# Performance work log

Hardware: AMD Instinct MI355X
Metric: run time of the kernel (lower is better)

The kernel has to match this reference:

```python
import jax, jax.numpy as jnp
import numpy as np
from jax.scipy.linalg import solve_triangular

JITTER = 1e-4  # settings.jitter
N, NUM_NODES, DIN, DOUT, M, DEG = 2048, 64, 4, 4, 128, 8
P = DEG * DIN  # parent-feature width per node


def _rbf(a, b):
    # unit-variance, unit-lengthscale RBF kernel: [Na, D] x [Nb, D] -> [Na, Nb]
    sq = (jnp.sum(a * a, -1)[:, None] + jnp.sum(b * b, -1)[None, :]
          - 2.0 * (a @ b.T))
    return jnp.exp(-0.5 * jnp.maximum(sq, 0.0))


def setup_inputs() -> dict:
    key = jax.random.key(0)
    k1, k2, k3, k4 = jax.random.split(key, 4)
    X = jax.random.normal(k1, (N, NUM_NODES * DIN), jnp.float32)
    Z = jax.random.normal(k2, (M, NUM_NODES * DIN), jnp.float32)
    q_mu = 0.1 * jax.random.normal(k3, (M, NUM_NODES * DOUT), jnp.float32)
    q_sqrt = (0.05 * jax.random.normal(k4, (NUM_NODES, DOUT, M, M), jnp.float32)
              + jnp.eye(M, dtype=jnp.float32))
    # fixed-degree graph: parents of node nd are (nd+k) % NUM_NODES, k<DEG;
    # pa[nd] holds the DIN contiguous feature columns of each parent (as in pa_idx)
    parents = (np.arange(NUM_NODES)[:, None] + np.arange(DEG)[None, :]) % NUM_NODES
    cols = (parents[:, :, None] * DIN + np.arange(DIN)[None, None, :]).reshape(NUM_NODES, P)
    pa = jnp.asarray(cols, dtype=jnp.int32)
    return {"X": X, "Z": Z, "q_mu": q_mu, "q_sqrt": q_sqrt, "pa": pa}


def reference(X, Z, q_mu, q_sqrt, pa):
    num_nodes, dout, m, _ = q_sqrt.shape
    n = X.shape[0]
    eye = jnp.eye(m, dtype=X.dtype)
    # q_mu columns per node: [M, nodes*Dout] -> [nodes, M, Dout]
    q_mu_n = q_mu.reshape(m, num_nodes, dout).transpose(1, 0, 2)

    def per_node(pa_nd, qmu_nd, qs_nd):
        Zn = Z[:, pa_nd]             # [M, P]
        Xn = X[:, pa_nd]             # [N, P]
        Ku = _rbf(Zn, Zn) + JITTER * eye
        Lu = jnp.linalg.cholesky(Ku)
        Kuf = _rbf(Zn, Xn)           # [M, N]
        A = solve_triangular(Lu, Kuf, lower=True)
        A = solve_triangular(Lu.T, A, lower=False)   # Kuu^{-1} Kuf, [M, N]
        mean = A.T @ qmu_nd          # [N, Dout] (Zero mean function)
        Lq = jnp.tril(qs_nd)         # [Dout, M, M]
        SK = jnp.einsum('dij,dkj->dik', Lq, Lq) - Ku[None]  # S - Kuu
        B = jnp.einsum('dmk,kn->dmn', SK, A)                 # [Dout, M, N]
        delta = jnp.einsum('mn,dmn->dn', A, B)               # [Dout, N]
        var = 1.0 + delta.T          # Kdiag of unit-variance RBF is 1
        return mean, var

    mean, var = jax.vmap(per_node)(pa, q_mu_n, q_sqrt)   # [nodes, N, Dout]
    mean = mean.transpose(1, 0, 2).reshape(n, num_nodes * dout)
    var = var.transpose(1, 0, 2).reshape(n, num_nodes * dout)
    return mean, var
```

## Files before the change

### kernel.cpp

```cpp
#include <hip/hip_runtime.h>
#include <hip/hip_bf16.h>

#define NN      2048
#define NODES   64
#define DIN     4
#define DOUT    4
#define MM      128
#define DEG     8
#define PP      32
#define JITTER  1e-4f

typedef __attribute__((ext_vector_type(8))) short short8;
typedef __attribute__((ext_vector_type(4))) float f32x4;
typedef __attribute__((ext_vector_type(4))) unsigned short bf16x4;

#define HSTRIDE 98304

__device__ __forceinline__ unsigned short f2b(float f) {
    union { float f; unsigned int u; } v; v.f = f;
    unsigned int u = v.u;
    u += 0x7fffu + ((u >> 16) & 1u);
    return (unsigned short)(u >> 16);
}
__device__ __forceinline__ float b2f(unsigned short h) {
    union { unsigned int u; float f; } v; v.u = ((unsigned int)h) << 16;
    return v.f;
}
__device__ __forceinline__ short8 pack8(f32x4 a, f32x4 b, float& sq) {
    short8 r;
    #pragma unroll
    for (int e = 0; e < 4; e++) {
        unsigned short ha = f2b(a[e]), hb = f2b(b[e]);
        float fa = b2f(ha), fb = b2f(hb);
        sq += fa * fa + fb * fb;
        r[e] = (short)ha; r[e + 4] = (short)hb;
    }
    return r;
}

__device__ __forceinline__ void gload16(const unsigned short* g, unsigned short* l) {
    __builtin_amdgcn_global_load_lds(
        (const __attribute__((address_space(1))) unsigned int*)g,
        (__attribute__((address_space(3))) unsigned int*)l, 16, 0, 0);
}

__global__ __launch_bounds__(512) void k_ns(const float* __restrict__ Z,
                                            const int* __restrict__ pa,
                                            const float* __restrict__ qmu,
                                            unsigned short* __restrict__ Wbf,
                                            unsigned short* __restrict__ Hbuf,
                                            unsigned short* __restrict__ Zpan,
                                            float* __restrict__ zsqg) {
    __shared__ unsigned short As[16384];
    __shared__ unsigned short Bs[16384];
    __shared__ float zsqs[128];
    __shared__ int cols[32];
    int node = blockIdx.x, t = threadIdx.x;
    int wv = t >> 6, ln = t & 63;
    if (t < 32) cols[t] = pa[node * 32 + t];
    __syncthreads();

    int wmI = wv & 1, wnI = wv >> 1;
    int wm = wmI * 64, wn = wnI * 32;
    int lr = ln & 15, lk = ln >> 4;
    int cg0 = cols[lk * 8], cg1 = cols[lk * 8 + 4];

    short8 zv[4], xv[2];
    #pragma unroll
    for (int mi = 0; mi < 4; mi++) {
        int m = wm + mi * 16 + lr;
        float sq = 0.f;
        zv[mi] = pack8(*(const f32x4*)(Z + (size_t)m * 256 + cg0),
                       *(const f32x4*)(Z + (size_t)m * 256 + cg1), sq);
        sq += __shfl_xor(sq, 16);
        sq += __shfl_xor(sq, 32);
        if (lk == 0) zsqs[m] = sq;
        if (wnI == 0)
            *(short8*)(Zpan + (size_t)node * 4096 + (size_t)m * 32 + lk * 8) = zv[mi];
    }
    #pragma unroll
    for (int ni = 0; ni < 2; ni++) {
        int x = wn + ni * 16 + lr;
        float sq = 0.f;
        xv[ni] = pack8(*(const f32x4*)(Z + (size_t)x * 256 + cg0),
                       *(const f32x4*)(Z + (size_t)x * 256 + cg1), sq);
    }
    __syncthreads();
    if (t < 128) zsqg[node * 128 + t] = zsqs[t];

    f32x4 dacc[4][2] = {};
    #pragma unroll
    for (int mi = 0; mi < 4; mi++)
        #pragma unroll
        for (int ni = 0; ni < 2; ni++)
            dacc[mi][ni] = __builtin_amdgcn_mfma_f32_16x16x32_bf16(zv[mi], xv[ni], dacc[mi][ni], 0, 0, 0);

    #pragma unroll
    for (int mi = 0; mi < 4; mi++) {
        int mb = wm + mi * 16 + lk * 4;
        f32x4 zs4 = *(const f32x4*)(zsqs + mb);
        #pragma unroll
        for (int ni = 0; ni < 2; ni++) {
            int x = wn + ni * 16 + lr;
            float xs = zsqs[x];
            bf16x4 kv4;
            #pragma unroll
            for (int j = 0; j < 4; j++) {
                float sq = fmaxf(zs4[j] + xs - 2.0f * dacc[mi][ni][j], 0.0f);
                float v = (mb + j == x) ? JITTER : __expf(-0.5f * sq);
                kv4[j] = f2b(v);
            }
            *(bf16x4*)(As + x * 128 + (((mb >> 3) ^ (x & 7)) * 8) + (mb & 7)) = kv4;
        }
    }
    __syncthreads();

    f32x4 acc1[4][2] = {};
    #pragma unroll
    for (int ks = 0; ks < 4; ks++) {
        int seg = ks * 4 + lk;
        short8 av[4], bv[2];
        #pragma unroll
        for (int mi = 0; mi < 4; mi++) {
            int r = wm + mi * 16 + lr;
            av[mi] = *(const short8*)(As + r * 128 + ((seg ^ (r & 7)) * 8));
        }
        #pragma unroll
        for (int ni = 0; ni < 2; ni++) {
            int x = wn + ni * 16 + lr;
            bv[ni] = *(const short8*)(As + x * 128 + ((seg ^ (x & 7)) * 8));
        }
        #pragma unroll
        for (int mi = 0; mi < 4; mi++)
            #pragma unroll
            for (int ni = 0; ni < 2; ni++)
                acc1[mi][ni] = __builtin_amdgcn_mfma_f32_16x16x32_bf16(av[mi], bv[ni], acc1[mi][ni], 0, 0, 0);
    }
    #pragma unroll
    for (int mi = 0; mi < 4; mi++)
        #pragma unroll
        for (int ni = 0; ni < 2; ni++)
            #pragma unroll
            for (int j = 0; j < 4; j++) {
                int rr = wm + mi * 16 + lk * 4 + j;
                int cc = wn + ni * 16 + lr;
                Bs[rr * 128 + (((cc >> 3) ^ (rr & 7)) * 8) + (cc & 7)] = f2b(acc1[mi][ni][j]);
            }
    __syncthreads();

    f32x4 acc2[4][2] = {};
    #pragma unroll
    for (int ks = 0; ks < 4; ks++) {
        int seg = ks * 4 + lk;
        short8 av[4], bv[2];
        #pragma unroll
        for (int mi = 0; mi < 4; mi++) {
            int r = wm + mi * 16 + lr;
            av[mi] = *(const short8*)(As + r * 128 + ((seg ^ (r & 7)) * 8));
        }
        #pragma unroll
        for (int ni = 0; ni < 2; ni++) {
            int x = wn + ni * 16 + lr;
            bv[ni] = *(const short8*)(Bs + x * 128 + ((seg ^ (x & 7)) * 8));
        }
        #pragma unroll
        for (int mi = 0; mi < 4; mi++)
            #pragma unroll
            for (int ni = 0; ni < 2; ni++)
                acc2[mi][ni] = __builtin_amdgcn_mfma_f32_16x16x32_bf16(av[mi], bv[ni], acc2[mi][ni], 0, 0, 0);
    }
    __syncthreads();

    unsigned short* Hr = Hbuf + (size_t)node * HSTRIDE + 65536;
    unsigned short* Hk = Hbuf + (size_t)node * HSTRIDE + 81920;
    #pragma unroll
    for (int mi = 0; mi < 4; mi++)
        #pragma unroll
        for (int ni = 0; ni < 2; ni++)
            #pragma unroll
            for (int j = 0; j < 4; j++) {
                int rr = wm + mi * 16 + lk * 4 + j;
                int cc = wn + ni * 16 + lr;
                int sw = rr * 128 + (((cc >> 3) ^ (rr & 7)) * 8) + (cc & 7);
                float dv = b2f(As[sw]);
                float eye = (rr == cc) ? 1.0f : 0.0f;
                float s1 = acc1[mi][ni][j], s2 = acc2[mi][ni][j];
                float kinv = eye - dv + s1 - s2;
                float rv = eye - 0.5f * dv + 0.375f * s1 - 0.3125f * s2;
                unsigned short kb = f2b(kinv);
                Hk[sw] = kb;
                As[sw] = kb;
                Hr[sw] = f2b(rv);
            }
    for (int q = t; q < 2048; q += 512) {
        int d = q >> 7, mm = q & 127;
        unsigned short val = 0;
        if (d < 4) val = f2b(qmu[mm * 256 + node * 4 + d]);
        Bs[d * 128 + (((mm >> 3) ^ (d & 7)) * 8) + (mm & 7)] = val;
    }
    __syncthreads();

    f32x4 wacc = {};
    #pragma unroll
    for (int ks = 0; ks < 4; ks++) {
        int seg = ks * 4 + lk;
        short8 aq = *(const short8*)(Bs + lr * 128 + ((seg ^ (lr & 7)) * 8));
        int x = wv * 16 + lr;
        short8 bk = *(const short8*)(As + x * 128 + ((seg ^ (x & 7)) * 8));
        wacc = __builtin_amdgcn_mfma_f32_16x16x32_bf16(aq, bk, wacc, 0, 0, 0);
    }
    unsigned short* Wg = Wbf + (size_t)node * 2048;
    #pragma unroll
    for (int j = 0; j < 4; j++) {
        int dd = lk * 4 + j;
        int mm = wv * 16 + lr;
        Wg[dd * 128 + (((mm >> 3) ^ (dd & 7)) * 8) + (mm & 7)] = f2b(wacc[j]);
    }
}

__global__ __launch_bounds__(256, 2) void k_gt(const unsigned short* __restrict__ Hbuf,
                                               const float* __restrict__ qsqrt,
                                               unsigned short* __restrict__ HbufOut) {
    __shared__ unsigned short Als[16384];
    __shared__ unsigned short Bls[16384];
    int bid = blockIdx.x, t = threadIdx.x;
    int node = (bid & 7) + 8 * (bid >> 5);
    int d = (bid >> 3) & 3;
    int wv = t >> 6, ln = t & 63;

    const unsigned short* Ksrc = Hbuf + (size_t)node * HSTRIDE + 81920;
    #pragma unroll
    for (int i = 0; i < 8; i++) {
        int ch = i * 4 + wv;
        gload16(Ksrc + ch * 512 + ln * 8, Bls + ch * 512);
    }
    const float* Lq = qsqrt + (size_t)(node * 4 + d) * 16384;
    int m = t & 127, ph = t >> 7;
    for (int pp = 0; pp < 64; pp++) {
        int p = ph * 64 + pp;
        float v = 0.f;
        if (p >= m) v = Lq[p * 128 + m];
        Als[m * 128 + (((p >> 3) ^ (m & 7)) * 8) + (p & 7)] = f2b(v);
    }
    __syncthreads();

    int wmI = wv & 1, wnI = wv >> 1;
    int wm = wmI * 64, wn = wnI * 64;
    int lr = ln & 15, lk = ln >> 4;
    f32x4 acc[4][4] = {};
    #pragma unroll
    for (int ks = 0; ks < 4; ks++) {
        int seg = ks * 4 + lk;
        short8 av[4], bv[4];
        #pragma unroll
        for (int mi = 0; mi < 4; mi++) {
            int r = wm + mi * 16 + lr;
            av[mi] = *(const short8*)(Als + r * 128 + ((seg ^ (r & 7)) * 8));
        }
        #pragma unroll
        for (int ni = 0; ni < 4; ni++) {
            int x = wn + ni * 16 + lr;
            bv[ni] = *(const short8*)(Bls + x * 128 + ((seg ^ (x & 7)) * 8));
        }
        #pragma unroll
        for (int mi = 0; mi < 4; mi++)
            #pragma unroll
            for (int ni = 0; ni < 4; ni++)
                acc[mi][ni] = __builtin_amdgcn_mfma_f32_16x16x32_bf16(av[mi], bv[ni], acc[mi][ni], 0, 0, 0);
    }
    unsigned short* Gg = HbufOut + (size_t)node * HSTRIDE + (size_t)d * 16384;
    #pragma unroll
    for (int mi = 0; mi < 4; mi++)
        #pragma unroll
        for (int ni = 0; ni < 4; ni++)
            #pragma unroll
            for (int j = 0; j < 4; j++) {
                int rr = wm + mi * 16 + lk * 4 + j;
                int cc = wn + ni * 16 + lr;
                Gg[rr * 128 + (((cc >> 3) ^ (rr & 7)) * 8) + (cc & 7)] = f2b(acc[mi][ni][j]);
            }
}

__global__ __launch_bounds__(512, 1) void k_main(const float* __restrict__ X,
                                                 const unsigned short* __restrict__ Zpan,
                                                 const float* __restrict__ zsqg,
                                                 const int* __restrict__ pa,
                                                 const unsigned short* __restrict__ Hbuf,
                                                 const unsigned short* __restrict__ Wbf,
                                                 float* __restrict__ out) {
    __shared__ unsigned short A0[16384];
    __shared__ unsigned short A1[16384];

    int bid = blockIdx.x;
    int node = (bid & 7) + 8 * (bid >> 6);
    int half = (bid >> 3) & 7;
    int x0 = half * 256;
    int t = threadIdx.x;
    int wv = t >> 6, ln = t & 63;
    int lr = ln & 15, lk = ln >> 4;

    const unsigned short* Asrc = Hbuf + (size_t)node * HSTRIDE;
    const unsigned short* Wsrc = Wbf + (size_t)node * 2048;
    int cg0 = pa[node * 32 + lk * 8];
    int cg1 = pa[node * 32 + lk * 8 + 4];

    unsigned short* strip = A1 + wv * 2048;

    const unsigned short* Zp = Zpan + (size_t)node * 4096;
    short8 zv[8];
    #pragma unroll
    for (int mi = 0; mi < 8; mi++)
        zv[mi] = *(const short8*)(Zp + (size_t)(mi * 16 + lr) * 32 + lk * 8);
    #pragma unroll
    for (int i = 0; i < 4; i++) {
        int ch = i * 8 + wv;
        gload16(Asrc + ch * 512 + ln * 8, A0 + ch * 512);
    }
    short8 aw[4];
    #pragma unroll
    for (int ks = 0; ks < 4; ks++)
        aw[ks] = *(const short8*)(Wsrc + lr * 128 + (((ks * 4 + lk) ^ (lr & 7)) * 8));

    const float* Xb = X + (size_t)(x0 + wv * 32 + lr) * 256;
    const float* zsq_n = zsqg + node * 128;
    f32x4 xr0 = *(const f32x4*)(Xb + cg0);
    f32x4 xr1 = *(const f32x4*)(Xb + cg1);
    short8 bvAll[2][4];
    f32x4 maccA[2];
    #pragma unroll
    for (int it = 0; it < 2; it++) {
        float xs = 0.f;
        short8 xv = pack8(xr0, xr1, xs);
        xs += __shfl_xor(xs, 16);
        xs += __shfl_xor(xs, 32);
        if (it < 1) {
            xr0 = *(const f32x4*)(Xb + 4096 + cg0);
            xr1 = *(const f32x4*)(Xb + 4096 + cg1);
        }
        f32x4 dacc[8] = {};
        #pragma unroll
        for (int mi = 0; mi < 8; mi++)
            dacc[mi] = __builtin_amdgcn_mfma_f32_16x16x32_bf16(zv[mi], xv, dacc[mi], 0, 0, 0);
        #pragma unroll
        for (int mi = 0; mi < 8; mi++) {
            int mb = mi * 16 + lk * 4;
            f32x4 zs4 = *(const f32x4*)(zsq_n + mb);
            bf16x4 kv4;
            #pragma unroll
            for (int j = 0; j < 4; j++) {
                float sq = fmaxf(zs4[j] + xs - 2.0f * dacc[mi][j], 0.0f);
                kv4[j] = f2b(__expf(-0.5f * sq));
            }
            *(bf16x4*)(strip + lr * 128 + (((mb >> 3) ^ (lr & 7)) * 8) + (mb & 7)) = kv4;
        }
        #pragma unroll
        for (int ks = 0; ks < 4; ks++)
            bvAll[it][ks] = *(const short8*)(strip + lr * 128 + (((ks * 4 + lk) ^ (lr & 7)) * 8));
        f32x4 m4 = {};
        #pragma unroll
        for (int ks = 0; ks < 4; ks++)
            m4 = __builtin_amdgcn_mfma_f32_16x16x32_bf16(aw[ks], bvAll[it][ks], m4, 0, 0, 0);
        maccA[it] = m4;
    }

    float vout[5][2];
    #pragma unroll
    for (int tt = 0; tt < 5; tt++) {
        unsigned short* cbuf = (tt & 1) ? A1 : A0;
        __syncthreads();
        if (tt < 4) {
            const unsigned short* ns = Asrc + (size_t)(tt + 1) * 16384;
            unsigned short* nb = (tt & 1) ? A0 : A1;
            #pragma unroll
            for (int i = 0; i < 4; i++) {
                int ch = i * 8 + wv;
                gload16(ns + ch * 512 + ln * 8, nb + ch * 512);
            }
        }
        float ssum[2] = {0.f, 0.f};
        __builtin_amdgcn_s_setprio(1);
        #pragma unroll
        for (int mi = 0; mi < 8; mi++) {
            int r = mi * 16 + lr;
            f32x4 a4[2] = {};
            #pragma unroll
            for (int ks = 0; ks < 4; ks++) {
                short8 av = *(const short8*)(cbuf + r * 128 + (((ks * 4 + lk) ^ (r & 7)) * 8));
                #pragma unroll
                for (int it = 0; it < 2; it++)
                    a4[it] = __builtin_amdgcn_mfma_f32_16x16x32_bf16(av, bvAll[it][ks], a4[it], 0, 0, 0);
            }
            #pragma unroll
            for (int it = 0; it < 2; it++)
                #pragma unroll
                for (int j = 0; j < 4; j++) ssum[it] += a4[it][j] * a4[it][j];
        }
        __builtin_amdgcn_s_setprio(0);
        #pragma unroll
        for (int it = 0; it < 2; it++) {
            float sv = ssum[it];
            sv += __shfl_xor(sv, 16);
            sv += __shfl_xor(sv, 32);
            vout[tt][it] = sv;
        }
    }

    if (lk == 0) {
        #pragma unroll
        for (int it = 0; it < 2; it++) {
            int x = x0 + wv * 32 + it * 16 + lr;
            f32x4 mv, vv;
            #pragma unroll
            for (int j = 0; j < 4; j++) {
                mv[j] = maccA[it][j];
                vv[j] = 1.0f + vout[j][it] - vout[4][it];
            }
            *(f32x4*)(out + (size_t)x * 256 + node * 4) = mv;
            *(f32x4*)(out + 524288 + (size_t)x * 256 + node * 4) = vv;
        }
    }
}

extern "C" void kernel_launch(void* const* d_in, const int* in_sizes, int n_in,
                              void* d_out, int out_size, void* d_ws, size_t ws_size,
                              hipStream_t stream) {
    const float* X = (const float*)d_in[0];
    const float* Z = (const float*)d_in[1];
    const float* qmu = (const float*)d_in[2];
    const float* qsqrt = (const float*)d_in[3];
    const int* pa = (const int*)d_in[4];
    float* out = (float*)d_out;

    char* ws = (char*)d_ws;
    size_t off = 0;
    unsigned short* Wbf = (unsigned short*)(ws + off);   off += 131072ull * 2;
    unsigned short* Hbuf = (unsigned short*)(ws + off);  off += 6291456ull * 2;
    unsigned short* Zpan = (unsigned short*)(ws + off);  off += 262144ull * 2;
    float* zsqg = (float*)(ws + off);                    off += 8192ull * 4;

    k_ns<<<64, 512, 0, stream>>>(Z, pa, qmu, Wbf, Hbuf, Zpan, zsqg);
    k_gt<<<256, 256, 0, stream>>>(Hbuf, qsqrt, Hbuf);
    k_main<<<512, 512, 0, stream>>>(X, Zpan, zsqg, pa, Hbuf, Wbf, out);
}
```

Measured before the change: 67.42 us.

## Fuse Kuu-inverse and Lq·Kinv kernels into one per-(node,d) kernel

Merges k_ns and k_gt into k_nsgt launched with 256 blocks, one per (node, output dim). Each block recomputes the Kuu inverse approximation and keeps it in shared memory, then multiplies it by the triangular Lq block directly. This removes the global round-trip of Kinv, the Hk buffer and one kernel launch, and spreads the prologue over more blocks. The cost is that the Kuu construction and Newton-Schulz steps are computed four times per node.

New measurement: 57.20 us. 15.2% less time.

```diff
diff --git a/kernel.cpp b/kernel.cpp
--- a/kernel.cpp
+++ b/kernel.cpp
@@ -14,7 +14,7 @@
 typedef __attribute__((ext_vector_type(4))) float f32x4;
 typedef __attribute__((ext_vector_type(4))) unsigned short bf16x4;
 
-#define HSTRIDE 98304
+#define HSTRIDE 81920
 
 __device__ __forceinline__ unsigned short f2b(float f) {
     union { float f; unsigned int u; } v; v.f = f;
@@ -44,18 +44,21 @@
         (__attribute__((address_space(3))) unsigned int*)l, 16, 0, 0);
 }
 
-__global__ __launch_bounds__(512) void k_ns(const float* __restrict__ Z,
-                                            const int* __restrict__ pa,
-                                            const float* __restrict__ qmu,
-                                            unsigned short* __restrict__ Wbf,
-                                            unsigned short* __restrict__ Hbuf,
-                                            unsigned short* __restrict__ Zpan,
-                                            float* __restrict__ zsqg) {
-    __shared__ unsigned short As[16384];
-    __shared__ unsigned short Bs[16384];
+__global__ __launch_bounds__(512) void k_nsgt(const float* __restrict__ Z,
+                                              const int* __restrict__ pa,
+                                              const float* __restrict__ qmu,
+                                              const float* __restrict__ qsqrt,
+                                              unsigned short* __restrict__ Wbf,
+                                              unsigned short* __restrict__ Hbuf,
+                                              unsigned short* __restrict__ Zpan,
+                                              float* __restrict__ zsqg) {
+    __shared__ unsigned short SA[16384];
+    __shared__ unsigned short SB[16384];
     __shared__ float zsqs[128];
     __shared__ int cols[32];
-    int node = blockIdx.x, t = threadIdx.x;
+    int bid = blockIdx.x, t = threadIdx.x;
+    int node = (bid & 7) + 8 * (bid >> 5);
+    int d = (bid >> 3) & 3;
     int wv = t >> 6, ln = t & 63;
     if (t < 32) cols[t] = pa[node * 32 + t];
     __syncthreads();
@@ -75,7 +78,7 @@
         sq += __shfl_xor(sq, 16);
         sq += __shfl_xor(sq, 32);
         if (lk == 0) zsqs[m] = sq;
-        if (wnI == 0)
+        if (d == 0 && wnI == 0)
             *(short8*)(Zpan + (size_t)node * 4096 + (size_t)m * 32 + lk * 8) = zv[mi];
     }
     #pragma unroll
@@ -86,7 +89,7 @@
                        *(const f32x4*)(Z + (size_t)x * 256 + cg1), sq);
     }
     __syncthreads();
-    if (t < 128) zsqg[node * 128 + t] = zsqs[t];
+    if (d == 0 && t < 128) zsqg[node * 128 + t] = zsqs[t];
 
     f32x4 dacc[4][2] = {};
     #pragma unroll
@@ -110,7 +113,7 @@
                 float v = (mb + j == x) ? JITTER : __expf(-0.5f * sq);
                 kv4[j] = f2b(v);
             }
-            *(bf16x4*)(As + x * 128 + (((mb >> 3) ^ (x & 7)) * 8) + (mb & 7)) = kv4;
+            *(bf16x4*)(SA + x * 128 + (((mb >> 3) ^ (x & 7)) * 8) + (mb & 7)) = kv4;
         }
     }
     __syncthreads();
@@ -123,12 +126,12 @@
         #pragma unroll
         for (int mi = 0; mi < 4; mi++) {
             int r = wm + mi * 16 + lr;
-            av[mi] = *(const short8*)(As + r * 128 + ((seg ^ (r & 7)) * 8));
+            av[mi] = *(const short8*)(SA + r * 128 + ((seg ^ (r & 7)) * 8));
         }
         #pragma unroll
         for (int ni = 0; ni < 2; ni++) {
             int x = wn + ni * 16 + lr;
-            bv[ni] = *(const short8*)(As + x * 128 + ((seg ^ (x & 7)) * 8));
+            bv[ni] = *(const short8*)(SA + x * 128 + ((seg ^ (x & 7)) * 8));
         }
         #pragma unroll
         for (int mi = 0; mi < 4; mi++)
@@ -144,7 +147,7 @@
             for (int j = 0; j < 4; j++) {
                 int rr = wm + mi * 16 + lk * 4 + j;
                 int cc = wn + ni * 16 + lr;
-                Bs[rr * 128 + (((cc >> 3) ^ (rr & 7)) * 8) + (cc & 7)] = f2b(acc1[mi][ni][j]);
+                SB[rr * 128 + (((cc >> 3) ^ (rr & 7)) * 8) + (cc & 7)] = f2b(acc1[mi][ni][j]);
             }
     __syncthreads();
 
@@ -156,12 +159,12 @@
         #pragma unroll
         for (int mi = 0; mi < 4; mi++) {
             int r = wm + mi * 16 + lr;
-            av[mi] = *(const short8*)(As + r * 128 + ((seg ^ (r & 7)) * 8));
+            av[mi] = *(const short8*)(SA + r * 128 + ((seg ^ (r & 7)) * 8));
         }
         #pragma unroll
         for (int ni = 0; ni < 2; ni++) {
             int x = wn + ni * 16 + lr;
-            bv[ni] = *(const short8*)(Bs + x * 128 + ((seg ^ (x & 7)) * 8));
+            bv[ni] = *(const short8*)(SB + x * 128 + ((seg ^ (x & 7)) * 8));
         }
         #pragma unroll
         for (int mi = 0; mi < 4; mi++)
@@ -172,7 +175,6 @@
     __syncthreads();
 
     unsigned short* Hr = Hbuf + (size_t)node * HSTRIDE + 65536;
-    unsigned short* Hk = Hbuf + (size_t)node * HSTRIDE + 81920;
     #pragma unroll
     for (int mi = 0; mi < 4; mi++)
         #pragma unroll
@@ -182,102 +184,87 @@
                 int rr = wm + mi * 16 + lk * 4 + j;
                 int cc = wn + ni * 16 + lr;
                 int sw = rr * 128 + (((cc >> 3) ^ (rr & 7)) * 8) + (cc & 7);
-                float dv = b2f(As[sw]);
+                float dv = b2f(SA[sw]);
                 float eye = (rr == cc) ? 1.0f : 0.0f;
                 float s1 = acc1[mi][ni][j], s2 = acc2[mi][ni][j];
                 float kinv = eye - dv + s1 - s2;
                 float rv = eye - 0.5f * dv + 0.375f * s1 - 0.3125f * s2;
-                unsigned short kb = f2b(kinv);
-                Hk[sw] = kb;
-                As[sw] = kb;
-                Hr[sw] = f2b(rv);
-            }
-    for (int q = t; q < 2048; q += 512) {
-        int d = q >> 7, mm = q & 127;
-        unsigned short val = 0;
-        if (d < 4) val = f2b(qmu[mm * 256 + node * 4 + d]);
-        Bs[d * 128 + (((mm >> 3) ^ (d & 7)) * 8) + (mm & 7)] = val;
-    }
-    __syncthreads();
-
-    f32x4 wacc = {};
+                SA[sw] = f2b(kinv);
+                if (d == 0) Hr[sw] = f2b(rv);
+            }
+    if (d == 0) {
+        for (int q = t; q < 2048; q += 512) {
+            int dd = q >> 7, mm = q & 127;
+            unsigned short val = 0;
+            if (dd < 4) val = f2b(qmu[mm * 256 + node * 4 + dd]);
+            SB[dd * 128 + (((mm >> 3) ^ (dd & 7)) * 8) + (mm & 7)] = val;
+        }
+    }
+    __syncthreads();
+
+    if (d == 0) {
+        f32x4 wacc = {};
+        #pragma unroll
+        for (int ks = 0; ks < 4; ks++) {
+            int seg = ks * 4 + lk;
+            short8 aq = *(const short8*)(SB + lr * 128 + ((seg ^ (lr & 7)) * 8));
+            int x = wv * 16 + lr;
+            short8 bk = *(const short8*)(SA + x * 128 + ((seg ^ (x & 7)) * 8));
+            wacc = __builtin_amdgcn_mfma_f32_16x16x32_bf16(aq, bk, wacc, 0, 0, 0);
+        }
+        unsigned short* Wg = Wbf + (size_t)node * 2048;
+        #pragma unroll
+        for (int j = 0; j < 4; j++) {
+            int dd = lk * 4 + j;
+            int mm = wv * 16 + lr;
+            Wg[dd * 128 + (((mm >> 3) ^ (dd & 7)) * 8) + (mm & 7)] = f2b(wacc[j]);
+        }
+    }
+    __syncthreads();
+
+    {
+        const float* Lq = qsqrt + (size_t)(node * 4 + d) * 16384;
+        int m = t & 127, ph = t >> 7;
+        for (int pp = 0; pp < 32; pp++) {
+            int p = ph * 32 + pp;
+            float v = 0.f;
+            if (p >= m) v = Lq[p * 128 + m];
+            SB[m * 128 + (((p >> 3) ^ (m & 7)) * 8) + (p & 7)] = f2b(v);
+        }
+    }
+    __syncthreads();
+
+    f32x4 gacc[4][2] = {};
     #pragma unroll
     for (int ks = 0; ks < 4; ks++) {
         int seg = ks * 4 + lk;
-        short8 aq = *(const short8*)(Bs + lr * 128 + ((seg ^ (lr & 7)) * 8));
-        int x = wv * 16 + lr;
-        short8 bk = *(const short8*)(As + x * 128 + ((seg ^ (x & 7)) * 8));
-        wacc = __builtin_amdgcn_mfma_f32_16x16x32_bf16(aq, bk, wacc, 0, 0, 0);
-    }
-    unsigned short* Wg = Wbf + (size_t)node * 2048;
-    #pragma unroll
-    for (int j = 0; j < 4; j++) {
-        int dd = lk * 4 + j;
-        int mm = wv * 16 + lr;
-        Wg[dd * 128 + (((mm >> 3) ^ (dd & 7)) * 8) + (mm & 7)] = f2b(wacc[j]);
-    }
-}
-
-__global__ __launch_bounds__(256, 2) void k_gt(const unsigned short* __restrict__ Hbuf,
-                                               const float* __restrict__ qsqrt,
-                                               unsigned short* __restrict__ HbufOut) {
-    __shared__ unsigned short Als[16384];
-    __shared__ unsigned short Bls[16384];
-    int bid = blockIdx.x, t = threadIdx.x;
-    int node = (bid & 7) + 8 * (bid >> 5);
-    int d = (bid >> 3) & 3;
-    int wv = t >> 6, ln = t & 63;
-
-    const unsigned short* Ksrc = Hbuf + (size_t)node * HSTRIDE + 81920;
-    #pragma unroll
-    for (int i = 0; i < 8; i++) {
-        int ch = i * 4 + wv;
-        gload16(Ksrc + ch * 512 + ln * 8, Bls + ch * 512);
-    }
-    const float* Lq = qsqrt + (size_t)(node * 4 + d) * 16384;
-    int m = t & 127, ph = t >> 7;
-    for (int pp = 0; pp < 64; pp++) {
-        int p = ph * 64 + pp;
-        float v = 0.f;
-        if (p >= m) v = Lq[p * 128 + m];
-        Als[m * 128 + (((p >> 3) ^ (m & 7)) * 8) + (p & 7)] = f2b(v);
-    }
-    __syncthreads();
-
-    int wmI = wv & 1, wnI = wv >> 1;
-    int wm = wmI * 64, wn = wnI * 64;
-    int lr = ln & 15, lk = ln >> 4;
-    f32x4 acc[4][4] = {};
-    #pragma unroll
-    for (int ks = 0; ks < 4; ks++) {
-        int seg = ks * 4 + lk;
-        short8 av[4], bv[4];
+        short8 av[4], bv[2];
         #pragma unroll
         for (int mi = 0; mi < 4; mi++) {
             int r = wm + mi * 16 + lr;
-            av[mi] = *(const short8*)(Als + r * 128 + ((seg ^ (r & 7)) * 8));
-        }
-        #pragma unroll
-        for (int ni = 0; ni < 4; ni++) {
+            av[mi] = *(const short8*)(SB + r * 128 + ((seg ^ (r & 7)) * 8));
+        }
+        #pragma unroll
+        for (int ni = 0; ni < 2; ni++) {
             int x = wn + ni * 16 + lr;
-            bv[ni] = *(const short8*)(Bls + x * 128 + ((seg ^ (x & 7)) * 8));
+            bv[ni] = *(const short8*)(SA + x * 128 + ((seg ^ (x & 7)) * 8));
         }
         #pragma unroll
         for (int mi = 0; mi < 4; mi++)
             #pragma unroll
-            for (int ni = 0; ni < 4; ni++)
-                acc[mi][ni] = __builtin_amdgcn_mfma_f32_16x16x32_bf16(av[mi], bv[ni], acc[mi][ni], 0, 0, 0);
-    }
-    unsigned short* Gg = HbufOut + (size_t)node * HSTRIDE + (size_t)d * 16384;
+            for (int ni = 0; ni < 2; ni++)
+                gacc[mi][ni] = __builtin_amdgcn_mfma_f32_16x16x32_bf16(av[mi], bv[ni], gacc[mi][ni], 0, 0, 0);
+    }
+    unsigned short* Gg = Hbuf + (size_t)node * HSTRIDE + (size_t)d * 16384;
     #pragma unroll
     for (int mi = 0; mi < 4; mi++)
         #pragma unroll
-        for (int ni = 0; ni < 4; ni++)
+        for (int ni = 0; ni < 2; ni++)
             #pragma unroll
             for (int j = 0; j < 4; j++) {
                 int rr = wm + mi * 16 + lk * 4 + j;
                 int cc = wn + ni * 16 + lr;
-                Gg[rr * 128 + (((cc >> 3) ^ (rr & 7)) * 8) + (cc & 7)] = f2b(acc[mi][ni][j]);
+                Gg[rr * 128 + (((cc >> 3) ^ (rr & 7)) * 8) + (cc & 7)] = f2b(gacc[mi][ni][j]);
             }
 }
 
@@ -434,11 +421,10 @@
     char* ws = (char*)d_ws;
     size_t off = 0;
     unsigned short* Wbf = (unsigned short*)(ws + off);   off += 131072ull * 2;
-    unsigned short* Hbuf = (unsigned short*)(ws + off);  off += 6291456ull * 2;
+    unsigned short* Hbuf = (unsigned short*)(ws + off);  off += 5242880ull * 2;
     unsigned short* Zpan = (unsigned short*)(ws + off);  off += 262144ull * 2;
     float* zsqg = (float*)(ws + off);                    off += 8192ull * 4;
 
-    k_ns<<<64, 512, 0, stream>>>(Z, pa, qmu, Wbf, Hbuf, Zpan, zsqg);
-    k_gt<<<256, 256, 0, stream>>>(Hbuf, qsqrt, Hbuf);
+    k_nsgt<<<256, 512, 0, stream>>>(Z, pa, qmu, qsqrt, Wbf, Hbuf, Zpan, zsqg);
     k_main<<<512, 512, 0, stream>>>(X, Zpan, zsqg, pa, Hbuf, Wbf, out);
 }
```
